# Optimization experiments

Hardware: AMD Instinct MI355X
Metric: run time of the kernel (lower is better)

Reference implementation:

```python
import jax, jax.numpy as jnp
import numpy as np
from jax.ops import segment_sum

B = 4096      # graphs per side (= batch of triples)
NPG = 32      # nodes per graph
N = B * NPG   # total nodes per batched graph
EPG = 128     # edges per graph
E = B * EPG   # total edges per batched graph
D = 256       # emb_dim
D4 = D // 4   # gnn1 out dim


def setup_inputs() -> dict:
    key = jax.random.key(0)
    ks = jax.random.split(key, 16)
    base = jnp.repeat(jnp.arange(B, dtype=jnp.int32) * NPG, EPG)  # graph offsets per edge
    def edges(k1, k2):
        s = base + jax.random.randint(k1, (E,), 0, NPG, dtype=jnp.int32)
        d = base + jax.random.randint(k2, (E,), 0, NPG, dtype=jnp.int32)
        return s, d
    subj_src, subj_dst = edges(ks[0], ks[1])
    obj_src, obj_dst = edges(ks[2], ks[3])
    node_graph_ids = jnp.repeat(jnp.arange(B, dtype=jnp.int32), NPG)
    # negative sampling indices (precomputed randomness, as in _sample_batch_negative_triples)
    head_or_tail = jax.random.randint(ks[4], (B,), 0, 2, dtype=jnp.int32)
    random_rows = jax.random.permutation(ks[5], B).astype(jnp.int32)
    ar = jnp.arange(B, dtype=jnp.int32)
    corrupt_hidx = jnp.where(head_or_tail == 1, random_rows, ar)
    corrupt_tidx = jnp.where(head_or_tail == 0, random_rows, ar)
    s = 0.02
    p = lambda k, sh: jax.random.normal(k, sh, dtype=jnp.float32) * s
    return {
        "subj_node_embs": jax.random.normal(ks[6], (N, D), dtype=jnp.float32),
        "obj_node_embs": jax.random.normal(ks[7], (N, D), dtype=jnp.float32),
        "rel_tok_embs": jax.random.normal(ks[8], (B, D), dtype=jnp.float32),
        "subj_src": subj_src, "subj_dst": subj_dst,
        "obj_src": obj_src, "obj_dst": obj_dst,
        "node_graph_ids": node_graph_ids,
        "corrupt_hidx": corrupt_hidx, "corrupt_tidx": corrupt_tidx,
        "WO1": p(ks[9], (D4, D)), "bO1": jnp.zeros((D4,), jnp.float32),
        "WI1": p(ks[10], (D4, D)), "bI1": jnp.zeros((D4,), jnp.float32),
        "WO2": p(ks[11], (D, D4)), "bO2": jnp.zeros((D,), jnp.float32),
        "WI2": p(ks[12], (D, D4)), "bI2": jnp.zeros((D,), jnp.float32),
        "relW": p(ks[13], (D, D)), "relb": jnp.zeros((D,), jnp.float32),
    }


def _mean_agg(h, idx_from, idx_to, n):
    # mean over edges (idx_from -> idx_to) of h[idx_from], per destination node; 0 for isolated
    deg = segment_sum(jnp.ones((idx_from.shape[0],), h.dtype), idx_to, num_segments=n)
    s = segment_sum(jnp.take(h, idx_from, axis=0), idx_to, num_segments=n)
    return s / jnp.maximum(deg, 1.0)[:, None]


def _compgcn(src, dst, h, WO, bO, WI, bI):
    n = h.shape[0]
    ho = _mean_agg(h, src, dst, n)   # forward graph: mean of in-neighbor sources
    hi = _mean_agg(h, dst, src, n)   # reversed graph: mean of out-neighbor targets
    return (ho @ WO.T + bO) + (hi @ WI.T + bI)


def _graph_emb(src, dst, node_embs, gids, WO1, bO1, WI1, bI1, WO2, bO2, WI2, bI2):
    hn = jax.nn.relu(_compgcn(src, dst, node_embs, WO1, bO1, WI1, bI1))
    hn = jax.nn.relu(_compgcn(src, dst, hn, WO2, bO2, WI2, bI2))
    # mean readout per graph
    cnt = segment_sum(jnp.ones((hn.shape[0],), hn.dtype), gids, num_segments=B)
    return segment_sum(hn, gids, num_segments=B) / cnt[:, None]


def _dist(h, r, t):
    return jnp.linalg.norm(h + r - t, ord=2, axis=1)


def reference(subj_node_embs, obj_node_embs, rel_tok_embs,
              subj_src, subj_dst, obj_src, obj_dst, node_graph_ids,
              corrupt_hidx, corrupt_tidx,
              WO1, bO1, WI1, bI1, WO2, bO2, WI2, bI2, relW, relb):
    h_embs = _graph_emb(subj_src, subj_dst, subj_node_embs, node_graph_ids,
                        WO1, bO1, WI1, bI1, WO2, bO2, WI2, bI2)
    t_embs = _graph_emb(obj_src, obj_dst, obj_node_embs, node_graph_ids,
                        WO1, bO1, WI1, bI1, WO2, bO2, WI2, bI2)
    r_embs = jax.nn.relu(rel_tok_embs @ relW.T + relb)
    pos_scores = _dist(h_embs, r_embs, t_embs)
    neg_scores = _dist(h_embs[corrupt_hidx], r_embs, t_embs[corrupt_tidx])
    return pos_scores, neg_scores
```

## Files before the change

kernel.cpp:

```cpp
#include <hip/hip_runtime.h>
#include <hip/hip_bf16.h>

#define BGR 4096
#define DIM 256
#define NG  8
#define HS  257

#define OFF_EB 0
#define OFF_YT 16896
#define OFF_H1 27136
#define OFF_A2 31744
#define OFF_CW 40448

typedef __bf16 bf16x8 __attribute__((ext_vector_type(8)));
typedef __bf16 bf16x4 __attribute__((ext_vector_type(4)));
typedef float  f32x4  __attribute__((ext_vector_type(4)));

__device__ __forceinline__ unsigned short f2b(float f) {
  unsigned u = __builtin_bit_cast(unsigned, f);
  u = (u + 0x7FFFu + ((u >> 16) & 1u)) >> 16;
  return (unsigned short)u;
}

__device__ __forceinline__ bf16x4 cvt4(f32x4 c) {
  bf16x4 r;
  r[0] = (__bf16)c[0]; r[1] = (__bf16)c[1]; r[2] = (__bf16)c[2]; r[3] = (__bf16)c[3];
  return r;
}

__device__ __forceinline__ void lds_barrier() {
  asm volatile("s_waitcnt lgkmcnt(0)" ::: "memory");
  __builtin_amdgcn_s_barrier();
  __builtin_amdgcn_sched_barrier(0);
}

__global__ void wcvt_kernel(
    const float* __restrict__ WO1, const float* __restrict__ WI1,
    const float* __restrict__ WO2, const float* __restrict__ WI2,
    const float* __restrict__ bO1, const float* __restrict__ bI1,
    const float* __restrict__ bO2, const float* __restrict__ bI2,
    unsigned short* __restrict__ W1b, unsigned short* __restrict__ W2b,
    float* __restrict__ b1, float* __restrict__ b2)
{
  const int i = blockIdx.x * 256 + threadIdx.x;
  { int j = i >> 8, k = i & 255;
    float v = (j < 64) ? WO1[j * 256 + k] : WI1[(j - 64) * 256 + k];
    W1b[i] = f2b(v); }
  { int j = i >> 7, k = i & 127;
    float v = (k < 64) ? WO2[j * 64 + k] : WI2[j * 64 + (k - 64)];
    W2b[i] = f2b(v); }
  if (i < 64)  b1[i] = bO1[i] + bI1[i];
  if (i < 256) b2[i] = bO2[i] + bI2[i];
}

__global__ __launch_bounds__(256)
__attribute__((amdgpu_waves_per_eu(1, 2)))
void fused_kernel(
    const float* __restrict__ subj, const float* __restrict__ obj,
    const int* __restrict__ ssrc, const int* __restrict__ sdst,
    const int* __restrict__ osrc, const int* __restrict__ odst,
    const unsigned short* __restrict__ W1b, const unsigned short* __restrict__ W2b,
    const float* __restrict__ b1, const float* __restrict__ b2,
    float* __restrict__ gout)
{
  __shared__ __align__(16) unsigned char S[43008];
  const int t = threadIdx.x, w = t >> 6, l = t & 63;
  const int ln16 = l & 15, kg = l >> 4;
  const int gid0 = blockIdx.x * NG;

  float4 ev[8];
  int es = 0, ed = 0;
  {
    const int gid = gid0;
    const float* Eg = ((gid >> 12) ? obj : subj) + (size_t)(gid & (BGR - 1)) * 32 * DIM;
    #pragma unroll
    for (int i = 0; i < 8; i++)
      ev[i] = *(const float4*)(Eg + (w * 8 + i) * 256 + l * 4);
    if (t < 128) {
      es = (((gid >> 12) ? osrc : ssrc))[(gid & (BGR - 1)) * 128 + t] & 31;
      ed = (((gid >> 12) ? odst : sdst))[(gid & (BGR - 1)) * 128 + t] & 31;
    }
  }
  bf16x8 B0[8], B1[8];
  {
    const unsigned short* wb0 = W1b + ((2 * w) * 16 + ln16) * 256 + kg * 8;
    const unsigned short* wb1 = W1b + ((2 * w + 1) * 16 + ln16) * 256 + kg * 8;
    #pragma unroll
    for (int ks = 0; ks < 8; ks++) {
      B0[ks] = *(const bf16x8*)(wb0 + ks * 32);
      B1[ks] = *(const bf16x8*)(wb1 + ks * 32);
    }
  }
  bf16x8 AW[4][4];
  float4 b2v[4];
  #pragma unroll
  for (int q = 0; q < 4; q++) {
    const int mt = w * 4 + q;
    const unsigned short* wa = W2b + (mt * 16 + ln16) * 128 + kg * 8;
    #pragma unroll
    for (int ks = 0; ks < 4; ks++) AW[q][ks] = *(const bf16x8*)(wa + ks * 32);
    b2v[q] = *(const float4*)(b2 + mt * 16 + kg * 4);
  }
  const float b1j = b1[w * 16 + ln16];
  {
    unsigned* cw = (unsigned*)(S + OFF_CW);
    for (int i = t; i < 640; i += 256) cw[i] = 0;
  }
  __syncthreads();
  if (t < 128) {
    unsigned* cw = (unsigned*)(S + OFF_CW);
    atomicAdd(&cw[ed * 8 + (es >> 2)], 1u << ((es & 3) * 8));
    atomicAdd(&cw[256 + ed], 1u);
    atomicAdd(&cw[288 + es], 1u);
  }
  #pragma unroll
  for (int i = 0; i < 8; i++) {
    f32x4 tmp = {ev[i].x, ev[i].y, ev[i].z, ev[i].w};
    *(bf16x4*)(S + OFF_EB + (w * 8 + i) * 528 + l * 8) = cvt4(tmp);
  }
  if (NG > 1) {
    const int gid = gid0 + 1;
    const float* Eg = ((gid >> 12) ? obj : subj) + (size_t)(gid & (BGR - 1)) * 32 * DIM;
    #pragma unroll
    for (int i = 0; i < 8; i++)
      ev[i] = *(const float4*)(Eg + (w * 8 + i) * 256 + l * 4);
    if (t < 128) {
      es = (((gid >> 12) ? osrc : ssrc))[(gid & (BGR - 1)) * 128 + t] & 31;
      ed = (((gid >> 12) ? odst : sdst))[(gid & (BGR - 1)) * 128 + t] & 31;
    }
  }

  for (int g = 0; g < NG; g++) {
    unsigned* cwc = (unsigned*)(S + OFF_CW + (g & 1) * 1280);
    unsigned* cwn = (unsigned*)(S + OFF_CW + ((g + 1) & 1) * 1280);

    lds_barrier();

    {
      f32x4 a00 = {0,0,0,0}, a01 = {0,0,0,0}, a10 = {0,0,0,0}, a11 = {0,0,0,0};
      const unsigned char* ea = S + OFF_EB + ln16 * 528 + kg * 16;
      #pragma unroll
      for (int ks = 0; ks < 8; ks++) {
        bf16x8 A0 = *(const bf16x8*)(ea + ks * 64);
        bf16x8 A1 = *(const bf16x8*)(ea + 16 * 528 + ks * 64);
        a00 = __builtin_amdgcn_mfma_f32_16x16x32_bf16(A0, B0[ks], a00, 0, 0, 0);
        a01 = __builtin_amdgcn_mfma_f32_16x16x32_bf16(A0, B1[ks], a01, 0, 0, 0);
        a10 = __builtin_amdgcn_mfma_f32_16x16x32_bf16(A1, B0[ks], a10, 0, 0, 0);
        a11 = __builtin_amdgcn_mfma_f32_16x16x32_bf16(A1, B1[ks], a11, 0, 0, 0);
      }
      *(bf16x4*)(S + OFF_YT + ((2 * w) * 16 + ln16) * 80 + (kg * 4) * 2)          = cvt4(a00);
      *(bf16x4*)(S + OFF_YT + ((2 * w + 1) * 16 + ln16) * 80 + (kg * 4) * 2)      = cvt4(a01);
      *(bf16x4*)(S + OFF_YT + ((2 * w) * 16 + ln16) * 80 + (16 + kg * 4) * 2)     = cvt4(a10);
      *(bf16x4*)(S + OFF_YT + ((2 * w + 1) * 16 + ln16) * 80 + (16 + kg * 4) * 2) = cvt4(a11);
      if (g + 1 < NG) for (int i = t; i < 320; i += 256) cwn[i] = 0;
    }
    lds_barrier();

    if (g + 1 < NG) {
      #pragma unroll
      for (int i = 0; i < 8; i++) {
        f32x4 tmp = {ev[i].x, ev[i].y, ev[i].z, ev[i].w};
        *(bf16x4*)(S + OFF_EB + (w * 8 + i) * 528 + l * 8) = cvt4(tmp);
      }
      if (t < 128) {
        atomicAdd(&cwn[ed * 8 + (es >> 2)], 1u << ((es & 3) * 8));
        atomicAdd(&cwn[256 + ed], 1u);
        atomicAdd(&cwn[288 + es], 1u);
      }
      if (g + 2 < NG) {
        const int ngid = gid0 + g + 2, ngg = ngid & (BGR - 1);
        const float* Eg = ((ngid >> 12) ? obj : subj) + (size_t)ngg * 32 * DIM;
        #pragma unroll
        for (int i = 0; i < 8; i++)
          ev[i] = *(const float4*)(Eg + (w * 8 + i) * 256 + l * 4);
        if (t < 128) {
          es = (((ngid >> 12) ? osrc : ssrc))[ngg * 128 + t] & 31;
          ed = (((ngid >> 12) ? odst : sdst))[ngg * 128 + t] & 31;
        }
      }
    }

    bf16x8 m1f[2], m2f[2];
    #pragma unroll
    for (int hf = 0; hf < 2; hf++) {
      const int r = hf * 16 + ln16;
      const float fi = 1.0f / fmaxf((float)cwc[256 + r], 1.0f);
      const float fo = 1.0f / fmaxf((float)cwc[288 + r], 1.0f);
      const unsigned w0 = cwc[r * 8 + kg * 2], w1 = cwc[r * 8 + kg * 2 + 1];
      bf16x8 a, b;
      #pragma unroll
      for (int q = 0; q < 4; q++) {
        a[q]     = (__bf16)((float)((w0 >> (q * 8)) & 255u) * fi);
        a[4 + q] = (__bf16)((float)((w1 >> (q * 8)) & 255u) * fi);
      }
      #pragma unroll
      for (int q = 0; q < 8; q++) {
        const unsigned wq = cwc[(kg * 8 + q) * 8 + (r >> 2)];
        b[q] = (__bf16)((float)((wq >> ((r & 3) * 8)) & 255u) * fo);
      }
      m1f[hf] = a; m2f[hf] = b;
    }
    {
      bf16x8 Byo = *(const bf16x8*)(S + OFF_YT + (w * 16 + ln16) * 80 + kg * 16);
      bf16x8 Byi = *(const bf16x8*)(S + OFF_YT + (64 + w * 16 + ln16) * 80 + kg * 16);
      #pragma unroll
      for (int mt = 0; mt < 2; mt++) {
        f32x4 z = {0.f, 0.f, 0.f, 0.f};
        f32x4 c = __builtin_amdgcn_mfma_f32_16x16x32_bf16(m1f[mt], Byo, z, 0, 0, 0);
        c = __builtin_amdgcn_mfma_f32_16x16x32_bf16(m2f[mt], Byi, c, 0, 0, 0);
        f32x4 hv = { fmaxf(c[0] + b1j, 0.f), fmaxf(c[1] + b1j, 0.f),
                     fmaxf(c[2] + b1j, 0.f), fmaxf(c[3] + b1j, 0.f) };
        *(bf16x4*)(S + OFF_H1 + (w * 16 + ln16) * 72 + (mt * 16 + kg * 4) * 2) = cvt4(hv);
      }
    }

    {
      bf16x8 Af = *(const bf16x8*)(S + OFF_H1 + (w * 16 + ln16) * 72 + kg * 16);
      #pragma unroll
      for (int hf = 0; hf < 2; hf++)
        #pragma unroll
        for (int ntd = 0; ntd < 2; ntd++) {
          f32x4 z = {0.f, 0.f, 0.f, 0.f};
          f32x4 c = __builtin_amdgcn_mfma_f32_16x16x32_bf16(
              Af, hf ? m2f[ntd] : m1f[ntd], z, 0, 0, 0);
          *(bf16x4*)(S + OFF_A2 + (ntd * 16 + ln16) * 272 + hf * 128 + w * 32 + kg * 8) = cvt4(c);
        }
    }
    lds_barrier();

    {
      bf16x8 BF[2][4];
      #pragma unroll
      for (int ntd = 0; ntd < 2; ntd++)
        #pragma unroll
        for (int ks = 0; ks < 4; ks++)
          BF[ntd][ks] = *(const bf16x8*)(S + OFF_A2 + (ntd * 16 + ln16) * 272 + ks * 64 + kg * 16);
      #pragma unroll
      for (int q = 0; q < 4; q++) {
        const int mt = w * 4 + q;
        f32x4 a0 = {0.f, 0.f, 0.f, 0.f}, a1 = {0.f, 0.f, 0.f, 0.f};
        #pragma unroll
        for (int ks = 0; ks < 4; ks++) {
          a0 = __builtin_amdgcn_mfma_f32_16x16x32_bf16(AW[q][ks], BF[0][ks], a0, 0, 0, 0);
          a1 = __builtin_amdgcn_mfma_f32_16x16x32_bf16(AW[q][ks], BF[1][ks], a1, 0, 0, 0);
        }
        float v0 = fmaxf(a0[0] + b2v[q].x, 0.f) + fmaxf(a1[0] + b2v[q].x, 0.f);
        float v1 = fmaxf(a0[1] + b2v[q].y, 0.f) + fmaxf(a1[1] + b2v[q].y, 0.f);
        float v2 = fmaxf(a0[2] + b2v[q].z, 0.f) + fmaxf(a1[2] + b2v[q].z, 0.f);
        float v3 = fmaxf(a0[3] + b2v[q].w, 0.f) + fmaxf(a1[3] + b2v[q].w, 0.f);
        #pragma unroll
        for (int d = 1; d < 16; d <<= 1) {
          v0 += __shfl_xor(v0, d); v1 += __shfl_xor(v1, d);
          v2 += __shfl_xor(v2, d); v3 += __shfl_xor(v3, d);
        }
        if (ln16 == 0) {
          float4 o = { v0 * 0.03125f, v1 * 0.03125f, v2 * 0.03125f, v3 * 0.03125f };
          *(float4*)(gout + (size_t)(gid0 + g) * DIM + mt * 16 + kg * 4) = o;
        }
      }
    }
  }
}

__global__ __launch_bounds__(256, 4) void rel_kernel(
    const float* __restrict__ rel, const float* __restrict__ relW,
    const float* __restrict__ relb, float* __restrict__ r_out)
{
  __shared__ float srel[16 * HS];
  const int t = threadIdx.x;
  const int b0 = blockIdx.x << 4;
  #pragma unroll
  for (int i = 0; i < 4; i++) {
    int f = (i << 8) + t;
    int r = f >> 6, k4 = f & 63;
    float4 x = *(const float4*)(rel + (size_t)(b0 + r) * DIM + (k4 << 2));
    float* d = &srel[r * HS + (k4 << 2)];
    d[0] = x.x; d[1] = x.y; d[2] = x.z; d[3] = x.w;
  }
  __syncthreads();
  const int r = t & 15, jg = t >> 4;
  const float* pa = &srel[r * HS];
  const float* w = relW + (size_t)(jg * 16) * DIM;
  float acc[16];
  #pragma unroll
  for (int jj = 0; jj < 16; jj++) acc[jj] = 0.f;
  for (int k0 = 0; k0 < DIM; k0 += 16) {
    float a[16];
    #pragma unroll
    for (int u = 0; u < 16; u++) a[u] = pa[k0 + u];
    #pragma unroll
    for (int jj = 0; jj < 16; jj++) {
      const float* wr = w + jj * DIM + k0;
      #pragma unroll
      for (int u = 0; u < 16; u += 4) {
        float4 wv = *(const float4*)(wr + u);
        acc[jj] += a[u]*wv.x + a[u+1]*wv.y + a[u+2]*wv.z + a[u+3]*wv.w;
      }
    }
  }
  float* outp = r_out + (size_t)(b0 + r) * DIM + jg * 16;
  #pragma unroll
  for (int jj = 0; jj < 16; jj++) outp[jj] = fmaxf(acc[jj] + relb[jg * 16 + jj], 0.f);
}

__global__ __launch_bounds__(256) void dist_kernel(
    const float* __restrict__ hemb, const float* __restrict__ temb,
    const float* __restrict__ remb, const int* __restrict__ chx,
    const int* __restrict__ ctx, float* __restrict__ out)
{
  const int t = threadIdx.x;
  const int w = t >> 6, l = t & 63;
  const int b = (blockIdx.x << 2) + w;
  float4 h4 = *(const float4*)(hemb + (size_t)b * DIM + (l << 2));
  float4 r4 = *(const float4*)(remb + (size_t)b * DIM + (l << 2));
  float4 t4 = *(const float4*)(temb + (size_t)b * DIM + (l << 2));
  int hb = chx[b], tb = ctx[b];
  float4 hn = *(const float4*)(hemb + (size_t)hb * DIM + (l << 2));
  float4 tn = *(const float4*)(temb + (size_t)tb * DIM + (l << 2));
  float x0 = h4.x + r4.x - t4.x, x1 = h4.y + r4.y - t4.y;
  float x2 = h4.z + r4.z - t4.z, x3 = h4.w + r4.w - t4.w;
  float dp = x0*x0 + x1*x1 + x2*x2 + x3*x3;
  float y0 = hn.x + r4.x - tn.x, y1 = hn.y + r4.y - tn.y;
  float y2 = hn.z + r4.z - tn.z, y3 = hn.w + r4.w - tn.w;
  float dn = y0*y0 + y1*y1 + y2*y2 + y3*y3;
  #pragma unroll
  for (int off = 32; off >= 1; off >>= 1) {
    dp += __shfl_down(dp, off);
    dn += __shfl_down(dn, off);
  }
  if (l == 0) {
    out[b] = sqrtf(dp);
    out[BGR + b] = sqrtf(dn);
  }
}

extern "C" void kernel_launch(void* const* d_in, const int* in_sizes, int n_in,
                              void* d_out, int out_size, void* d_ws, size_t ws_size,
                              hipStream_t stream) {
  const float* subj_embs = (const float*)d_in[0];
  const float* obj_embs  = (const float*)d_in[1];
  const float* rel_tok   = (const float*)d_in[2];
  const int* subj_src = (const int*)d_in[3];
  const int* subj_dst = (const int*)d_in[4];
  const int* obj_src  = (const int*)d_in[5];
  const int* obj_dst  = (const int*)d_in[6];
  const int* chx = (const int*)d_in[8];
  const int* ctx = (const int*)d_in[9];
  const float* WO1 = (const float*)d_in[10];
  const float* bO1 = (const float*)d_in[11];
  const float* WI1 = (const float*)d_in[12];
  const float* bI1 = (const float*)d_in[13];
  const float* WO2 = (const float*)d_in[14];
  const float* bO2 = (const float*)d_in[15];
  const float* WI2 = (const float*)d_in[16];
  const float* bI2 = (const float*)d_in[17];
  const float* relW = (const float*)d_in[18];
  const float* relb = (const float*)d_in[19];

  float* g_embs = (float*)d_ws;
  float* r_embs = g_embs + (size_t)2 * BGR * DIM;
  unsigned short* W1b = (unsigned short*)((char*)d_ws + 12582912);
  unsigned short* W2b = W1b + 32768;
  float* b1 = (float*)((char*)d_ws + 12713984);
  float* b2 = b1 + 64;
  float* out = (float*)d_out;

  wcvt_kernel<<<128, 256, 0, stream>>>(WO1, WI1, WO2, WI2, bO1, bI1, bO2, bI2,
                                       W1b, W2b, b1, b2);
  fused_kernel<<<8192 / NG, 256, 0, stream>>>(
      subj_embs, obj_embs, subj_src, subj_dst, obj_src, obj_dst,
      W1b, W2b, b1, b2, g_embs);
  rel_kernel<<<BGR / 16, 256, 0, stream>>>(rel_tok, relW, relb, r_embs);
  dist_kernel<<<BGR / 4, 256, 0, stream>>>(
      g_embs, g_embs + (size_t)BGR * DIM, r_embs, chx, ctx, out);
}
```

Before: 206.5 us.

## Merge weight conversion and relation GEMM into one GNN mega-kernel

Drops the separate weight-conversion kernel. Each GNN block now loads the fp32 weights and converts them to bf16 in registers. The relation projection becomes extra blocks of the same launch, which overlaps the rel GEMM with the graph work and saves two kernel launches. Graphs per block double from 8 to 16, giving 512 GNN blocks, which amortizes the weight loads but leaves fewer blocks to spread across CUs. Every GNN block now reads fp32 weights (twice the bytes) and converts them redundantly.

```diff
diff --git a/kernel.cpp b/kernel.cpp
--- a/kernel.cpp
+++ b/kernel.cpp
@@ -3,7 +3,8 @@
 
 #define BGR 4096
 #define DIM 256
-#define NG  8
+#define NG  16
+#define NFUSED 512
 #define HS  257
 
 #define OFF_EB 0
@@ -16,12 +17,12 @@
 typedef __bf16 bf16x4 __attribute__((ext_vector_type(4)));
 typedef float  f32x4  __attribute__((ext_vector_type(4)));
 
-__device__ __forceinline__ unsigned short f2b(float f) {
-  unsigned u = __builtin_bit_cast(unsigned, f);
-  u = (u + 0x7FFFu + ((u >> 16) & 1u)) >> 16;
-  return (unsigned short)u;
-}
-
+__device__ __forceinline__ bf16x8 cvt8(float4 a, float4 b) {
+  bf16x8 r;
+  r[0] = (__bf16)a.x; r[1] = (__bf16)a.y; r[2] = (__bf16)a.z; r[3] = (__bf16)a.w;
+  r[4] = (__bf16)b.x; r[5] = (__bf16)b.y; r[6] = (__bf16)b.z; r[7] = (__bf16)b.w;
+  return r;
+}
 __device__ __forceinline__ bf16x4 cvt4(f32x4 c) {
   bf16x4 r;
   r[0] = (__bf16)c[0]; r[1] = (__bf16)c[1]; r[2] = (__bf16)c[2]; r[3] = (__bf16)c[3];
@@ -34,37 +35,63 @@
   __builtin_amdgcn_sched_barrier(0);
 }
 
-__global__ void wcvt_kernel(
+__global__ __launch_bounds__(256)
+__attribute__((amdgpu_waves_per_eu(1, 2)))
+void mega_kernel(
+    const float* __restrict__ subj, const float* __restrict__ obj,
+    const int* __restrict__ ssrc, const int* __restrict__ sdst,
+    const int* __restrict__ osrc, const int* __restrict__ odst,
     const float* __restrict__ WO1, const float* __restrict__ WI1,
     const float* __restrict__ WO2, const float* __restrict__ WI2,
     const float* __restrict__ bO1, const float* __restrict__ bI1,
     const float* __restrict__ bO2, const float* __restrict__ bI2,
-    unsigned short* __restrict__ W1b, unsigned short* __restrict__ W2b,
-    float* __restrict__ b1, float* __restrict__ b2)
-{
-  const int i = blockIdx.x * 256 + threadIdx.x;
-  { int j = i >> 8, k = i & 255;
-    float v = (j < 64) ? WO1[j * 256 + k] : WI1[(j - 64) * 256 + k];
-    W1b[i] = f2b(v); }
-  { int j = i >> 7, k = i & 127;
-    float v = (k < 64) ? WO2[j * 64 + k] : WI2[j * 64 + (k - 64)];
-    W2b[i] = f2b(v); }
-  if (i < 64)  b1[i] = bO1[i] + bI1[i];
-  if (i < 256) b2[i] = bO2[i] + bI2[i];
-}
-
-__global__ __launch_bounds__(256)
-__attribute__((amdgpu_waves_per_eu(1, 2)))
-void fused_kernel(
-    const float* __restrict__ subj, const float* __restrict__ obj,
-    const int* __restrict__ ssrc, const int* __restrict__ sdst,
-    const int* __restrict__ osrc, const int* __restrict__ odst,
-    const unsigned short* __restrict__ W1b, const unsigned short* __restrict__ W2b,
-    const float* __restrict__ b1, const float* __restrict__ b2,
-    float* __restrict__ gout)
+    const float* __restrict__ rel, const float* __restrict__ relW,
+    const float* __restrict__ relb,
+    float* __restrict__ gout, float* __restrict__ r_out)
 {
   __shared__ __align__(16) unsigned char S[43008];
-  const int t = threadIdx.x, w = t >> 6, l = t & 63;
+  const int t = threadIdx.x;
+
+  if (blockIdx.x >= NFUSED) {
+    float* srel = (float*)S;
+    const int b0 = (blockIdx.x - NFUSED) << 4;
+    #pragma unroll
+    for (int i = 0; i < 4; i++) {
+      int f = (i << 8) + t;
+      int r = f >> 6, k4 = f & 63;
+      float4 x = *(const float4*)(rel + (size_t)(b0 + r) * DIM + (k4 << 2));
+      float* d = &srel[r * HS + (k4 << 2)];
+      d[0] = x.x; d[1] = x.y; d[2] = x.z; d[3] = x.w;
+    }
+    __syncthreads();
+    const int r = t & 15, jg = t >> 4;
+    const float* pa = &srel[r * HS];
+    const float* wr0 = relW + (size_t)(jg * 16) * DIM;
+    float acc[16];
+    #pragma unroll
+    for (int jj = 0; jj < 16; jj++) acc[jj] = 0.f;
+    for (int k0 = 0; k0 < DIM; k0 += 16) {
+      float a[16];
+      #pragma unroll
+      for (int u = 0; u < 16; u++) a[u] = pa[k0 + u];
+      #pragma unroll
+      for (int jj = 0; jj < 16; jj++) {
+        const float* wrr = wr0 + jj * DIM + k0;
+        #pragma unroll
+        for (int u = 0; u < 16; u += 4) {
+          float4 wv = *(const float4*)(wrr + u);
+          acc[jj] += a[u]*wv.x + a[u+1]*wv.y + a[u+2]*wv.z + a[u+3]*wv.w;
+        }
+      }
+    }
+    float* outp = r_out + (size_t)(b0 + r) * DIM + jg * 16;
+    #pragma unroll
+    for (int jj = 0; jj < 16; jj++)
+      outp[jj] = fmaxf(acc[jj] + relb[jg * 16 + jj], 0.f);
+    return;
+  }
+
+  const int w = t >> 6, l = t & 63;
   const int ln16 = l & 15, kg = l >> 4;
   const int gid0 = blockIdx.x * NG;
 
@@ -83,25 +110,35 @@
   }
   bf16x8 B0[8], B1[8];
   {
-    const unsigned short* wb0 = W1b + ((2 * w) * 16 + ln16) * 256 + kg * 8;
-    const unsigned short* wb1 = W1b + ((2 * w + 1) * 16 + ln16) * 256 + kg * 8;
+    const int j0 = (2 * w) * 16 + ln16, j1 = (2 * w + 1) * 16 + ln16;
+    const float* s0 = (j0 < 64) ? (WO1 + (size_t)j0 * 256) : (WI1 + (size_t)(j0 - 64) * 256);
+    const float* s1 = (j1 < 64) ? (WO1 + (size_t)j1 * 256) : (WI1 + (size_t)(j1 - 64) * 256);
     #pragma unroll
     for (int ks = 0; ks < 8; ks++) {
-      B0[ks] = *(const bf16x8*)(wb0 + ks * 32);
-      B1[ks] = *(const bf16x8*)(wb1 + ks * 32);
+      const int k = ks * 32 + kg * 8;
+      B0[ks] = cvt8(*(const float4*)(s0 + k), *(const float4*)(s0 + k + 4));
+      B1[ks] = cvt8(*(const float4*)(s1 + k), *(const float4*)(s1 + k + 4));
     }
   }
   bf16x8 AW[4][4];
   float4 b2v[4];
   #pragma unroll
   for (int q = 0; q < 4; q++) {
-    const int mt = w * 4 + q;
-    const unsigned short* wa = W2b + (mt * 16 + ln16) * 128 + kg * 8;
-    #pragma unroll
-    for (int ks = 0; ks < 4; ks++) AW[q][ks] = *(const bf16x8*)(wa + ks * 32);
-    b2v[q] = *(const float4*)(b2 + mt * 16 + kg * 4);
-  }
-  const float b1j = b1[w * 16 + ln16];
+    const int row = (w * 4 + q) * 16 + ln16;
+    const float* o2 = WO2 + (size_t)row * 64;
+    const float* i2 = WI2 + (size_t)row * 64;
+    #pragma unroll
+    for (int ks = 0; ks < 4; ks++) {
+      const int k = ks * 32 + kg * 8;
+      const float* sp = (k < 64) ? (o2 + k) : (i2 + (k - 64));
+      AW[q][ks] = cvt8(*(const float4*)(sp), *(const float4*)(sp + 4));
+    }
+    const int jb = (w * 4 + q) * 16 + kg * 4;
+    float4 bo = *(const float4*)(bO2 + jb);
+    float4 bi = *(const float4*)(bI2 + jb);
+    b2v[q] = make_float4(bo.x + bi.x, bo.y + bi.y, bo.z + bi.z, bo.w + bi.w);
+  }
+  const float b1j = bO1[w * 16 + ln16] + bI1[w * 16 + ln16];
   {
     unsigned* cw = (unsigned*)(S + OFF_CW);
     for (int i = t; i < 640; i += 256) cw[i] = 0;
@@ -260,47 +297,6 @@
       }
     }
   }
-}
-
-__global__ __launch_bounds__(256, 4) void rel_kernel(
-    const float* __restrict__ rel, const float* __restrict__ relW,
-    const float* __restrict__ relb, float* __restrict__ r_out)
-{
-  __shared__ float srel[16 * HS];
-  const int t = threadIdx.x;
-  const int b0 = blockIdx.x << 4;
-  #pragma unroll
-  for (int i = 0; i < 4; i++) {
-    int f = (i << 8) + t;
-    int r = f >> 6, k4 = f & 63;
-    float4 x = *(const float4*)(rel + (size_t)(b0 + r) * DIM + (k4 << 2));
-    float* d = &srel[r * HS + (k4 << 2)];
-    d[0] = x.x; d[1] = x.y; d[2] = x.z; d[3] = x.w;
-  }
-  __syncthreads();
-  const int r = t & 15, jg = t >> 4;
-  const float* pa = &srel[r * HS];
-  const float* w = relW + (size_t)(jg * 16) * DIM;
-  float acc[16];
-  #pragma unroll
-  for (int jj = 0; jj < 16; jj++) acc[jj] = 0.f;
-  for (int k0 = 0; k0 < DIM; k0 += 16) {
-    float a[16];
-    #pragma unroll
-    for (int u = 0; u < 16; u++) a[u] = pa[k0 + u];
-    #pragma unroll
-    for (int jj = 0; jj < 16; jj++) {
-      const float* wr = w + jj * DIM + k0;
-      #pragma unroll
-      for (int u = 0; u < 16; u += 4) {
-        float4 wv = *(const float4*)(wr + u);
-        acc[jj] += a[u]*wv.x + a[u+1]*wv.y + a[u+2]*wv.z + a[u+3]*wv.w;
-      }
-    }
-  }
-  float* outp = r_out + (size_t)(b0 + r) * DIM + jg * 16;
-  #pragma unroll
-  for (int jj = 0; jj < 16; jj++) outp[jj] = fmaxf(acc[jj] + relb[jg * 16 + jj], 0.f);
 }
 
 __global__ __launch_bounds__(256) void dist_kernel(
@@ -359,18 +355,12 @@
 
   float* g_embs = (float*)d_ws;
   float* r_embs = g_embs + (size_t)2 * BGR * DIM;
-  unsigned short* W1b = (unsigned short*)((char*)d_ws + 12582912);
-  unsigned short* W2b = W1b + 32768;
-  float* b1 = (float*)((char*)d_ws + 12713984);
-  float* b2 = b1 + 64;
   float* out = (float*)d_out;
 
-  wcvt_kernel<<<128, 256, 0, stream>>>(WO1, WI1, WO2, WI2, bO1, bI1, bO2, bI2,
-                                       W1b, W2b, b1, b2);
-  fused_kernel<<<8192 / NG, 256, 0, stream>>>(
+  mega_kernel<<<NFUSED + 256, 256, 0, stream>>>(
       subj_embs, obj_embs, subj_src, subj_dst, obj_src, obj_dst,
-      W1b, W2b, b1, b2, g_embs);
-  rel_kernel<<<BGR / 16, 256, 0, stream>>>(rel_tok, relW, relb, r_embs);
+      WO1, WI1, WO2, WI2, bO1, bI1, bO2, bI2,
+      rel_tok, relW, relb, g_embs, r_embs);
   dist_kernel<<<BGR / 4, 256, 0, stream>>>(
       g_embs, g_embs + (size_t)BGR * DIM, r_embs, chx, ctx, out);
 }
```

After: 182.2 us. 1.13x faster.

## Merge relation projection into the graph kernel and double graphs per block

Applied to the files above, without the earlier changes.

Folds the relation-embedding matmul into the fused graph kernel as extra trailing blocks, so it runs alongside the GNN work in one launch instead of as a separate kernel. It also raises graphs per block from 8 to 16, giving 512 GNN blocks instead of 1024. The goal is to save a launch, fill idle CUs with the relation work and amortise per-block setup. The risk is that the relation blocks now inherit the fused kernel's register and occupancy attributes, and fewer, larger GNN blocks may balance worse across CUs.

```diff
diff --git a/kernel.cpp b/kernel.cpp
--- a/kernel.cpp
+++ b/kernel.cpp
@@ -3,7 +3,8 @@
 
 #define BGR 4096
 #define DIM 256
-#define NG  8
+#define NG  16
+#define NFUSED 512
 #define HS  257
 
 #define OFF_EB 0
@@ -55,16 +56,59 @@
 
 __global__ __launch_bounds__(256)
 __attribute__((amdgpu_waves_per_eu(1, 2)))
-void fused_kernel(
+void mega_kernel(
     const float* __restrict__ subj, const float* __restrict__ obj,
     const int* __restrict__ ssrc, const int* __restrict__ sdst,
     const int* __restrict__ osrc, const int* __restrict__ odst,
     const unsigned short* __restrict__ W1b, const unsigned short* __restrict__ W2b,
     const float* __restrict__ b1, const float* __restrict__ b2,
-    float* __restrict__ gout)
+    const float* __restrict__ rel, const float* __restrict__ relW,
+    const float* __restrict__ relb,
+    float* __restrict__ gout, float* __restrict__ r_out)
 {
   __shared__ __align__(16) unsigned char S[43008];
-  const int t = threadIdx.x, w = t >> 6, l = t & 63;
+  const int t = threadIdx.x;
+
+  if (blockIdx.x >= NFUSED) {
+    float* srel = (float*)S;
+    const int b0 = (blockIdx.x - NFUSED) << 4;
+    #pragma unroll
+    for (int i = 0; i < 4; i++) {
+      int f = (i << 8) + t;
+      int r = f >> 6, k4 = f & 63;
+      float4 x = *(const float4*)(rel + (size_t)(b0 + r) * DIM + (k4 << 2));
+      float* d = &srel[r * HS + (k4 << 2)];
+      d[0] = x.x; d[1] = x.y; d[2] = x.z; d[3] = x.w;
+    }
+    __syncthreads();
+    const int r = t & 15, jg = t >> 4;
+    const float* pa = &srel[r * HS];
+    const float* wr0 = relW + (size_t)(jg * 16) * DIM;
+    float acc[16];
+    #pragma unroll
+    for (int jj = 0; jj < 16; jj++) acc[jj] = 0.f;
+    for (int k0 = 0; k0 < DIM; k0 += 16) {
+      float a[16];
+      #pragma unroll
+      for (int u = 0; u < 16; u++) a[u] = pa[k0 + u];
+      #pragma unroll
+      for (int jj = 0; jj < 16; jj++) {
+        const float* wrr = wr0 + jj * DIM + k0;
+        #pragma unroll
+        for (int u = 0; u < 16; u += 4) {
+          float4 wv = *(const float4*)(wrr + u);
+          acc[jj] += a[u]*wv.x + a[u+1]*wv.y + a[u+2]*wv.z + a[u+3]*wv.w;
+        }
+      }
+    }
+    float* outp = r_out + (size_t)(b0 + r) * DIM + jg * 16;
+    #pragma unroll
+    for (int jj = 0; jj < 16; jj++)
+      outp[jj] = fmaxf(acc[jj] + relb[jg * 16 + jj], 0.f);
+    return;
+  }
+
+  const int w = t >> 6, l = t & 63;
   const int ln16 = l & 15, kg = l >> 4;
   const int gid0 = blockIdx.x * NG;
 
@@ -260,47 +304,6 @@
       }
     }
   }
-}
-
-__global__ __launch_bounds__(256, 4) void rel_kernel(
-    const float* __restrict__ rel, const float* __restrict__ relW,
-    const float* __restrict__ relb, float* __restrict__ r_out)
-{
-  __shared__ float srel[16 * HS];
-  const int t = threadIdx.x;
-  const int b0 = blockIdx.x << 4;
-  #pragma unroll
-  for (int i = 0; i < 4; i++) {
-    int f = (i << 8) + t;
-    int r = f >> 6, k4 = f & 63;
-    float4 x = *(const float4*)(rel + (size_t)(b0 + r) * DIM + (k4 << 2));
-    float* d = &srel[r * HS + (k4 << 2)];
-    d[0] = x.x; d[1] = x.y; d[2] = x.z; d[3] = x.w;
-  }
-  __syncthreads();
-  const int r = t & 15, jg = t >> 4;
-  const float* pa = &srel[r * HS];
-  const float* w = relW + (size_t)(jg * 16) * DIM;
-  float acc[16];
-  #pragma unroll
-  for (int jj = 0; jj < 16; jj++) acc[jj] = 0.f;
-  for (int k0 = 0; k0 < DIM; k0 += 16) {
-    float a[16];
-    #pragma unroll
-    for (int u = 0; u < 16; u++) a[u] = pa[k0 + u];
-    #pragma unroll
-    for (int jj = 0; jj < 16; jj++) {
-      const float* wr = w + jj * DIM + k0;
-      #pragma unroll
-      for (int u = 0; u < 16; u += 4) {
-        float4 wv = *(const float4*)(wr + u);
-        acc[jj] += a[u]*wv.x + a[u+1]*wv.y + a[u+2]*wv.z + a[u+3]*wv.w;
-      }
-    }
-  }
-  float* outp = r_out + (size_t)(b0 + r) * DIM + jg * 16;
-  #pragma unroll
-  for (int jj = 0; jj < 16; jj++) outp[jj] = fmaxf(acc[jj] + relb[jg * 16 + jj], 0.f);
 }
 
 __global__ __launch_bounds__(256) void dist_kernel(
@@ -367,10 +370,9 @@
 
   wcvt_kernel<<<128, 256, 0, stream>>>(WO1, WI1, WO2, WI2, bO1, bI1, bO2, bI2,
                                        W1b, W2b, b1, b2);
-  fused_kernel<<<8192 / NG, 256, 0, stream>>>(
+  mega_kernel<<<NFUSED + 256, 256, 0, stream>>>(
       subj_embs, obj_embs, subj_src, subj_dst, obj_src, obj_dst,
-      W1b, W2b, b1, b2, g_embs);
-  rel_kernel<<<BGR / 16, 256, 0, stream>>>(rel_tok, relW, relb, r_embs);
+      W1b, W2b, b1, b2, rel_tok, relW, relb, g_embs, r_embs);
   dist_kernel<<<BGR / 4, 256, 0, stream>>>(
       g_embs, g_embs + (size_t)BGR * DIM, r_embs, chx, ctx, out);
 }
```

New measurement: 178.6 us, median of 2. 1.16x faster.
